# Optimization experiments

Measured on AMD Instinct MI355X. Metric: run time of the kernel, lower is better.

Reference implementation:

```python
import jax, jax.numpy as jnp
import numpy as np

N_NODES = 50000
N_EDGES = 600000
HIDDEN = 128
N_FEAT = 1
N_CLASSES = 2
N_GRAPHS = 500


def gcn_conv(x, W, b, src, dst, n_nodes):
    # PyG GCNConv: add self-loops, symmetric normalization deg^{-1/2} A_hat deg^{-1/2}, then XW + b
    h = x @ W  # [N, out]
    deg = jnp.zeros((n_nodes,), h.dtype).at[dst].add(1.0) + 1.0  # +1 for self-loop
    dinv = jax.lax.rsqrt(deg)
    norm = dinv[src] * dinv[dst]  # [E]
    agg = jax.ops.segment_sum(h[src] * norm[:, None], dst, num_segments=n_nodes)
    # self-loop contribution: norm_ii = dinv_i^2
    agg = agg + h * (dinv * dinv)[:, None]
    return agg + b


def setup_inputs() -> dict:
    key = jax.random.key(0)
    ks = jax.random.split(key, 12)
    x = jax.random.normal(ks[0], (N_NODES, N_FEAT), dtype=jnp.float32)
    edge_index = jax.random.randint(ks[1], (2, N_EDGES), 0, N_NODES, dtype=jnp.int64)
    batch = jnp.sort(jax.random.randint(ks[2], (N_NODES,), 0, N_GRAPHS, dtype=jnp.int64))

    def glorot(k, fan_in, fan_out):
        lim = np.sqrt(6.0 / (fan_in + fan_out)).astype(np.float32)
        return jax.random.uniform(k, (fan_in, fan_out), jnp.float32, -lim, lim)

    W1 = glorot(ks[3], N_FEAT, HIDDEN)
    b1 = jnp.zeros((HIDDEN,), jnp.float32)
    W2 = glorot(ks[4], HIDDEN, HIDDEN)
    b2 = jnp.zeros((HIDDEN,), jnp.float32)
    W3 = glorot(ks[5], HIDDEN, HIDDEN)
    b3 = jnp.zeros((HIDDEN,), jnp.float32)
    Wlin = glorot(ks[6], HIDDEN, N_CLASSES)
    blin = jnp.zeros((N_CLASSES,), jnp.float32)
    return {"x": x, "W1": W1, "b1": b1, "W2": W2, "b2": b2, "W3": W3,
            "b3": b3, "Wlin": Wlin, "blin": blin,
            "edge_index": edge_index, "batch": batch}


def reference(x, W1, b1, W2, b2, W3, b3, Wlin, blin, edge_index, batch):
    src, dst = edge_index[0], edge_index[1]
    n = x.shape[0]
    h = jax.nn.relu(gcn_conv(x, W1, b1, src, dst, n))
    h = jax.nn.relu(gcn_conv(h, W2, b2, src, dst, n))
    h = gcn_conv(h, W3, b3, src, dst, n)
    # global mean pool over graphs
    sums = jax.ops.segment_sum(h, batch, num_segments=N_GRAPHS)
    counts = jax.ops.segment_sum(jnp.ones((n,), h.dtype), batch, num_segments=N_GRAPHS)
    pooled = sums / jnp.maximum(counts, 1.0)[:, None]  # [G, HIDDEN]
    # dropout is identity in eval mode
    return pooled @ Wlin + blin  # [G, N_CLASSES]
```

## Files before the change

kernel.cpp:

```cpp
#include <hip/hip_runtime.h>

#define N_NODES 50000
#define N_EDGES 600000
#define HID     128
#define NG      500
#define MAXDEG  48
#define ECAP    664
#define NEB     147
#define NBUCK   782
#define BCAP    1024

typedef __attribute__((ext_vector_type(8))) short short8;
typedef __attribute__((ext_vector_type(4))) float f32x4;

static __device__ __forceinline__ ushort f2bf(float f) {
    uint u = __float_as_uint(f);
    return (ushort)((u + 0x7fffu + ((u >> 16) & 1u)) >> 16);
}
static __device__ __forceinline__ float bf2f(ushort h) {
    return __uint_as_float(((uint)h) << 16);
}


__global__ __launch_bounds__(256) void k_bin(const int* __restrict__ src,
                                             const int* __restrict__ dst,
                                             int* __restrict__ gcnt,
                                             uint* __restrict__ ebuf,
                                             const float* __restrict__ W2,
                                             const float* __restrict__ W3,
                                             const float* __restrict__ Wlin,
                                             const float* __restrict__ b3,
                                             const float* __restrict__ blin,
                                             const int* __restrict__ batch,
                                             float* __restrict__ w3buf,
                                             ushort* __restrict__ w2fh,
                                             ushort* __restrict__ w2fl,
                                             int* __restrict__ starts) {
    if (blockIdx.x >= NEB) {
        int t = threadIdx.x;
        if (blockIdx.x == NEB) {
            int k = t >> 1, j = t & 1;
            float acc = 0.f;
            for (int m = 0; m < 128; m++) acc += W3[k * 128 + m] * Wlin[m * 2 + j];
            w3buf[k * 2 + j] = acc;
            if (t < 2) {
                float c = 0.f;
                for (int m = 0; m < 128; m++) c += b3[m] * Wlin[m * 2 + t];
                w3buf[256 + t] = c + blin[t];
                w3buf[258 + t] = blin[t];
            }
            for (int g = t; g <= NG; g += 256) {
                int lo = 0, hi = N_NODES;
                while (lo < hi) { int mid = (lo + hi) >> 1; if (batch[mid] < g) lo = mid + 1; else hi = mid; }
                starts[g] = lo;
            }
        } else {
            int q = blockIdx.x - (NEB + 1);
            for (int idx = q * 4096 + t; idx < (q + 1) * 4096; idx += 256) {
                int nt = idx >> 11, kt = (idx >> 9) & 3, ln = (idx >> 3) & 63, i = idx & 7;
                int k = kt * 32 + (ln >> 4) * 8 + i;
                int col = nt * 16 + (ln & 15);
                float v = W2[k * 128 + col];
                ushort h = f2bf(v);
                w2fh[idx] = h;
                w2fl[idx] = f2bf(v - bf2f(h));
            }
        }
        return;
    }
    __shared__ int lcnt[NBUCK];
    __shared__ int gbase[NBUCK];
    int t = threadIdx.x;
    for (int i = t; i < NBUCK; i += 256) lcnt[i] = 0;
    __syncthreads();
    uint pk[16];
    uint blp[16];
    const int4* s4 = (const int4*)src;
    const int4* d4 = (const int4*)dst;
    int b4 = blockIdx.x * 1024;
    #pragma unroll
    for (int u = 0; u < 4; u++) {
        int i4 = b4 + u * 256 + t;
        if (i4 < N_EDGES / 4) {
            int4 dv = d4[i4], sv = s4[i4];
            int dd[4] = {dv.x, dv.y, dv.z, dv.w};
            int ss[4] = {sv.x, sv.y, sv.z, sv.w};
            #pragma unroll
            for (int j = 0; j < 4; j++) {
                int b = dd[j] >> 6;
                int p = atomicAdd(&lcnt[b], 1);
                pk[u * 4 + j]  = ((uint)ss[j] << 16) | (uint)(dd[j] & 63);
                blp[u * 4 + j] = ((uint)b << 12) | (uint)p;
            }
        } else {
            #pragma unroll
            for (int j = 0; j < 4; j++) blp[u * 4 + j] = 0xFFFFFFFFu;
        }
    }
    __syncthreads();
    for (int i = t; i < NBUCK; i += 256) {
        int c = lcnt[i];
        gbase[i] = c ? atomicAdd(&gcnt[i], c) : 0;
    }
    __syncthreads();
    #pragma unroll
    for (int u = 0; u < 16; u++) {
        if (blp[u] != 0xFFFFFFFFu) {
            int b = (int)(blp[u] >> 12);
            int slot = gbase[b] + (int)(blp[u] & 0xFFFu);
            if (slot < BCAP) ebuf[b * BCAP + slot] = pk[u];
        }
    }
}


__global__ __launch_bounds__(256) void k_place(const int* __restrict__ gcnt,
                                               const uint* __restrict__ ebuf,
                                               const float* __restrict__ x,
                                               int* __restrict__ ell,
                                               int* __restrict__ cnt,
                                               float* __restrict__ dinv,
                                               float* __restrict__ xd) {
    int b = blockIdx.x;
    __shared__ int lc[64];
    int t = threadIdx.x;
    if (t < 64) lc[t] = 0;
    __syncthreads();
    int n = min(gcnt[b], BCAP);
    int d0 = b << 6;
    for (int i = t; i < n; i += 256) {
        uint e = ebuf[b * BCAP + i];
        int dl = (int)(e & 63u);
        int s  = (int)(e >> 16);
        int p = atomicAdd(&lc[dl], 1);
        if (p < MAXDEG) ell[(d0 + dl) * MAXDEG + p] = s;
    }
    __syncthreads();
    if (t < 64) {
        int d = d0 + t;
        if (d < N_NODES) {
            int c = lc[t];
            cnt[d] = c;
            float di = rsqrtf((float)c + 1.0f);
            dinv[d] = di;
            xd[d] = x[d] * di;
        }
    }
}

__global__ void k_s1d(const float* __restrict__ xd, const float* __restrict__ dinv,
                      const int* __restrict__ cnt, const int* __restrict__ ell,
                      float2* __restrict__ s1d) {
    int tid = blockIdx.x * 256 + threadIdx.x;
    int i = tid >> 3, sub = tid & 7;
    if (i >= N_NODES) return;
    int c = min(cnt[i], MAXDEG);
    float acc = 0.f;
    for (int p = sub; p < c; p += 8) acc += xd[ell[i * MAXDEG + p]];
    acc += __shfl_xor(acc, 1);
    acc += __shfl_xor(acc, 2);
    acc += __shfl_xor(acc, 4);
    if (sub == 0) {
        float di = dinv[i];
        float2 r = {(xd[i] + acc) * di, di};
        s1d[i] = r;
    }
}


__global__ __launch_bounds__(256, 8) void k_gemm_fused(const float2* __restrict__ s1d,
                                                       const int* __restrict__ cnt,
                                                       const int* __restrict__ ell,
                                                       const float* __restrict__ W1,
                                                       const float* __restrict__ b1,
                                                       const ushort* __restrict__ w2fh,
                                                       const ushort* __restrict__ w2fl,
                                                       const float* __restrict__ b2,
                                                       const float* __restrict__ w3buf,
                                                       const float* __restrict__ dinv,
                                                       float* __restrict__ zd) {
    __shared__ __align__(16) ushort Hhi[32 * 136];
    __shared__ __align__(16) ushort Hlo[32 * 136];
    __shared__ float2 sjd_sh[ECAP];
    __shared__ int cnt_sh[32];
    __shared__ int pref_sh[33];
    int t = threadIdx.x;
    int r0 = blockIdx.x * 32;
    int lane = t & 31, grp = t >> 5;

    if (t < 32) {
        int i = r0 + t;
        int c = (i < N_NODES) ? min(cnt[i], MAXDEG) : 0;
        cnt_sh[t] = c;
        int inc = c;
        for (int o = 1; o < 32; o <<= 1) {
            int u = __shfl_up(inc, o);
            if (t >= o) inc += u;
        }
        pref_sh[t] = inc - c;
        if (t == 31) pref_sh[32] = inc;
    }
    __syncthreads();
    int total = pref_sh[32];
    bool fast = (total <= ECAP);
    if (fast) {
        #pragma unroll
        for (int u = 0; u < 6; u++) {
            int s = u * 256 + t;
            int ln = s / MAXDEG, p = s - ln * MAXDEG;
            if (p < cnt_sh[ln]) {
                int j = ell[(r0 + ln) * MAXDEG + p];
                sjd_sh[pref_sh[ln] + p] = s1d[j];
            }
        }
    }
    __syncthreads();

    float w1r[16], b1r[16];
    #pragma unroll
    for (int kk = 0; kk < 16; kk++) { w1r[kk] = W1[grp * 16 + kk]; b1r[kk] = b1[grp * 16 + kk]; }

    float ga[16];
    #pragma unroll
    for (int kk = 0; kk < 16; kk++) ga[kk] = 0.f;
    int node = r0 + lane;
    if (node < N_NODES) {
        float2 sd = s1d[node];
        float di = sd.y, wself = sd.y * sd.y;
        #pragma unroll
        for (int kk = 0; kk < 16; kk++) ga[kk] = fmaxf(sd.x * w1r[kk] + b1r[kk], 0.f) * wself;
        int c = cnt_sh[lane];
        if (fast) {
            const float2* myrow = &sjd_sh[pref_sh[lane]];
            int p = 0;
            for (; p + 3 < c; p += 4) {
                float2 s0 = myrow[p], s1v = myrow[p+1], s2 = myrow[p+2], s3 = myrow[p+3];
                float wj0 = s0.y * di, wj1 = s1v.y * di, wj2 = s2.y * di, wj3 = s3.y * di;
                #pragma unroll
                for (int kk = 0; kk < 16; kk++) {
                    ga[kk] += fmaxf(s0.x  * w1r[kk] + b1r[kk], 0.f) * wj0
                            + fmaxf(s1v.x * w1r[kk] + b1r[kk], 0.f) * wj1
                            + fmaxf(s2.x  * w1r[kk] + b1r[kk], 0.f) * wj2
                            + fmaxf(s3.x  * w1r[kk] + b1r[kk], 0.f) * wj3;
                }
            }
            for (; p < c; p++) {
                float2 sj = myrow[p];
                float wj = sj.y * di;
                #pragma unroll
                for (int kk = 0; kk < 16; kk++)
                    ga[kk] += fmaxf(sj.x * w1r[kk] + b1r[kk], 0.f) * wj;
            }
        } else {
            for (int p = 0; p < c; p++) {
                float2 sj = s1d[ell[node * MAXDEG + p]];
                float wj = sj.y * di;
                #pragma unroll
                for (int kk = 0; kk < 16; kk++)
                    ga[kk] += fmaxf(sj.x * w1r[kk] + b1r[kk], 0.f) * wj;
            }
        }
    }
    #pragma unroll
    for (int kk = 0; kk < 16; kk += 2) {
        int ch = grp * 16 + kk;
        ushort h0 = f2bf(ga[kk]);      ushort l0 = f2bf(ga[kk]     - bf2f(h0));
        ushort h1v = f2bf(ga[kk + 1]); ushort l1v = f2bf(ga[kk + 1] - bf2f(h1v));
        *(uint*)&Hhi[lane * 136 + ch] = (uint)h0 | ((uint)h1v << 16);
        *(uint*)&Hlo[lane * 136 + ch] = (uint)l0 | ((uint)l1v << 16);
    }
    __syncthreads();

    int wv = t >> 6, l = t & 63;
    int l15 = l & 15, lk = l >> 4;
    f32x4 acc00 = {0.f,0.f,0.f,0.f}, acc01 = {0.f,0.f,0.f,0.f};
    f32x4 acc10 = {0.f,0.f,0.f,0.f}, acc11 = {0.f,0.f,0.f,0.f};
    const short8* Bh = (const short8*)w2fh;
    const short8* Bl = (const short8*)w2fl;
    #pragma unroll
    for (int kt = 0; kt < 4; kt++) {
        int ao = l15 * 136 + kt * 32 + lk * 8;
        short8 ah0 = *(const short8*)&Hhi[ao];
        short8 ah1 = *(const short8*)&Hhi[ao + 16 * 136];
        short8 al0 = *(const short8*)&Hlo[ao];
        short8 al1 = *(const short8*)&Hlo[ao + 16 * 136];
        {
            int ng = 2 * wv;
            short8 bh = Bh[(ng * 4 + kt) * 64 + l];
            short8 bl = Bl[(ng * 4 + kt) * 64 + l];
            acc00 = __builtin_amdgcn_mfma_f32_16x16x32_bf16(ah0, bh, acc00, 0, 0, 0);
            acc00 = __builtin_amdgcn_mfma_f32_16x16x32_bf16(ah0, bl, acc00, 0, 0, 0);
            acc00 = __builtin_amdgcn_mfma_f32_16x16x32_bf16(al0, bh, acc00, 0, 0, 0);
            acc10 = __builtin_amdgcn_mfma_f32_16x16x32_bf16(ah1, bh, acc10, 0, 0, 0);
            acc10 = __builtin_amdgcn_mfma_f32_16x16x32_bf16(ah1, bl, acc10, 0, 0, 0);
            acc10 = __builtin_amdgcn_mfma_f32_16x16x32_bf16(al1, bh, acc10, 0, 0, 0);
        }
        {
            int ng = 2 * wv + 1;
            short8 bh = Bh[(ng * 4 + kt) * 64 + l];
            short8 bl = Bl[(ng * 4 + kt) * 64 + l];
            acc01 = __builtin_amdgcn_mfma_f32_16x16x32_bf16(ah0, bh, acc01, 0, 0, 0);
            acc01 = __builtin_amdgcn_mfma_f32_16x16x32_bf16(ah0, bl, acc01, 0, 0, 0);
            acc01 = __builtin_amdgcn_mfma_f32_16x16x32_bf16(al0, bh, acc01, 0, 0, 0);
            acc11 = __builtin_amdgcn_mfma_f32_16x16x32_bf16(ah1, bh, acc11, 0, 0, 0);
            acc11 = __builtin_amdgcn_mfma_f32_16x16x32_bf16(ah1, bl, acc11, 0, 0, 0);
            acc11 = __builtin_amdgcn_mfma_f32_16x16x32_bf16(al1, bh, acc11, 0, 0, 0);
        }
    }

    float p0[2][4], p1[2][4];
    #pragma unroll
    for (int mt = 0; mt < 2; mt++)
        #pragma unroll
        for (int r = 0; r < 4; r++) { p0[mt][r] = 0.f; p1[mt][r] = 0.f; }
    {
        int colg = (2 * wv) * 16 + l15;
        float b2c = b2[colg], w0 = w3buf[colg * 2], w1c = w3buf[colg * 2 + 1];
        #pragma unroll
        for (int r = 0; r < 4; r++) {
            float v0 = fmaxf(acc00[r] + b2c, 0.f);
            float v1 = fmaxf(acc10[r] + b2c, 0.f);
            p0[0][r] += v0 * w0; p1[0][r] += v0 * w1c;
            p0[1][r] += v1 * w0; p1[1][r] += v1 * w1c;
        }
    }
    {
        int colg = (2 * wv + 1) * 16 + l15;
        float b2c = b2[colg], w0 = w3buf[colg * 2], w1c = w3buf[colg * 2 + 1];
        #pragma unroll
        for (int r = 0; r < 4; r++) {
            float v0 = fmaxf(acc01[r] + b2c, 0.f);
            float v1 = fmaxf(acc11[r] + b2c, 0.f);
            p0[0][r] += v0 * w0; p1[0][r] += v0 * w1c;
            p0[1][r] += v1 * w0; p1[1][r] += v1 * w1c;
        }
    }
    #pragma unroll
    for (int o = 1; o < 16; o <<= 1) {
        #pragma unroll
        for (int mt = 0; mt < 2; mt++)
            #pragma unroll
            for (int r = 0; r < 4; r++) {
                p0[mt][r] += __shfl_xor(p0[mt][r], o);
                p1[mt][r] += __shfl_xor(p1[mt][r], o);
            }
    }
    float* zpart = (float*)sjd_sh;
    if (l15 == 0) {
        #pragma unroll
        for (int mt = 0; mt < 2; mt++)
            #pragma unroll
            for (int r = 0; r < 4; r++) {
                int row = mt * 16 + lk * 4 + r;
                zpart[(wv * 32 + row) * 2 + 0] = p0[mt][r];
                zpart[(wv * 32 + row) * 2 + 1] = p1[mt][r];
            }
    }
    __syncthreads();
    if (t < 64) {
        int row = t >> 1, o = t & 1;
        float s = zpart[row * 2 + o] + zpart[(32 + row) * 2 + o]
                + zpart[(64 + row) * 2 + o] + zpart[(96 + row) * 2 + o];
        int rg = r0 + row;
        if (rg < N_NODES) zd[rg * 2 + o] = s * dinv[rg];
    }
}


__global__ void k_aggz(const float* __restrict__ zd, const int* __restrict__ cnt,
                       const int* __restrict__ ell, const float* __restrict__ dinv,
                       const int* __restrict__ batch, float* __restrict__ gsum) {
    __shared__ float sa0[32], sa1[32];
    __shared__ int sg[32];
    int tid = blockIdx.x * 256 + threadIdx.x;
    int t = threadIdx.x;
    int i = tid >> 3, sub = tid & 7;
    const float2* Z = (const float2*)zd;
    float a0 = 0.f, a1 = 0.f;
    if (i < N_NODES) {
        int c = min(cnt[i], MAXDEG);
        for (int p = sub; p < c; p += 8) {
            float2 zj = Z[ell[i * MAXDEG + p]];
            a0 += zj.x; a1 += zj.y;
        }
    }
    a0 += __shfl_xor(a0, 1); a1 += __shfl_xor(a1, 1);
    a0 += __shfl_xor(a0, 2); a1 += __shfl_xor(a1, 2);
    a0 += __shfl_xor(a0, 4); a1 += __shfl_xor(a1, 4);
    if (sub == 0) {
        int li = t >> 3;
        if (i < N_NODES) {
            float di = dinv[i];
            float2 zi = Z[i];
            sa0[li] = (zi.x + a0) * di;
            sa1[li] = (zi.y + a1) * di;
            sg[li] = batch[i];
        } else { sa0[li] = 0.f; sa1[li] = 0.f; sg[li] = -1; }
    }
    __syncthreads();
    if (t < 32) {
        float v0 = sa0[t], v1 = sa1[t];
        int g = sg[t];
        #pragma unroll
        for (int o = 1; o < 32; o <<= 1) {
            float u0 = __shfl_up(v0, o), u1 = __shfl_up(v1, o);
            int ug = __shfl_up(g, o);
            if (t >= o && ug == g) { v0 += u0; v1 += u1; }
        }
        int gn = __shfl_down(g, 1);
        bool last = (t == 31) || (g != gn);
        if (last && g >= 0) {
            atomicAdd(&gsum[g * 2 + 0], v0);
            atomicAdd(&gsum[g * 2 + 1], v1);
        }
    }
}


__global__ __launch_bounds__(256) void k_final2(const float* __restrict__ gsum,
                                                const int* __restrict__ starts,
                                                const float* __restrict__ w3buf,
                                                float* __restrict__ out) {
    int t = threadIdx.x;
    for (int g = t; g < NG; g += 256) {
        int c = starts[g + 1] - starts[g];
        if (c > 0) {
            float inv = 1.0f / (float)c;
            out[g * 2 + 0] = gsum[g * 2 + 0] * inv + w3buf[256];
            out[g * 2 + 1] = gsum[g * 2 + 1] * inv + w3buf[257];
        } else {
            out[g * 2 + 0] = w3buf[258];
            out[g * 2 + 1] = w3buf[259];
        }
    }
}


extern "C" void kernel_launch(void* const* d_in, const int* in_sizes, int n_in,
                              void* d_out, int out_size, void* d_ws, size_t ws_size,
                              hipStream_t stream) {
    const float* x    = (const float*)d_in[0];
    const float* W1   = (const float*)d_in[1];
    const float* b1   = (const float*)d_in[2];
    const float* W2   = (const float*)d_in[3];
    const float* b2   = (const float*)d_in[4];
    const float* W3   = (const float*)d_in[5];
    const float* b3   = (const float*)d_in[6];
    const float* Wlin = (const float*)d_in[7];
    const float* blin = (const float*)d_in[8];
    const int*   eidx = (const int*)d_in[9];
    const int*   batch= (const int*)d_in[10];
    const int* esrc = eidx;
    const int* edst = eidx + N_EDGES;
    float* out = (float*)d_out;

    char* w = (char*)d_ws;
    size_t off = 0;
    auto alloc = [&](size_t bytes) { size_t o = off; off = (off + bytes + 255) & ~(size_t)255; return o; };
    int*   cnt    = (int*)  (w + alloc(N_NODES * 4));
    int*   ell    = (int*)  (w + alloc((size_t)N_NODES * MAXDEG * 4));
    float* dinv   = (float*)(w + alloc(N_NODES * 4));
    float* xd     = (float*)(w + alloc(N_NODES * 4));
    float2* s1d   = (float2*)(w + alloc((size_t)N_NODES * 8));
    float* w3buf  = (float*)(w + alloc(260 * 4));
    float* zd     = (float*)(w + alloc((size_t)N_NODES * 2 * 4));
    ushort* w2fh  = (ushort*)(w + alloc(16384 * 2));
    ushort* w2fl  = (ushort*)(w + alloc(16384 * 2));
    int*   starts = (int*)  (w + alloc((NG + 4) * 4));
    int*   gcnt   = (int*)  (w + alloc(NBUCK * 4));
    float* gsum   = (float*)(w + alloc(NG * 2 * 4));
    uint*  ebuf   = (uint*) (w + alloc((size_t)NBUCK * BCAP * 4));

    const int QB = (N_NODES * 8 + 255) / 256;
    size_t zbytes = (size_t)((char*)gsum - (char*)gcnt) + NG * 2 * 4;
    hipMemsetAsync(gcnt, 0, zbytes, stream);
    k_bin<<<NEB + 5, 256, 0, stream>>>(esrc, edst, gcnt, ebuf, W2, W3, Wlin, b3, blin,
                                       batch, w3buf, w2fh, w2fl, starts);
    k_place<<<NBUCK, 256, 0, stream>>>(gcnt, ebuf, x, ell, cnt, dinv, xd);
    k_s1d<<<QB, 256, 0, stream>>>(xd, dinv, cnt, ell, s1d);
    k_gemm_fused<<<(N_NODES + 31) / 32, 256, 0, stream>>>(s1d, cnt, ell,
                                                          W1, b1, w2fh, w2fl, b2, w3buf,
                                                          dinv, zd);
    k_aggz<<<QB, 256, 0, stream>>>(zd, cnt, ell, dinv, batch, gsum);
    k_final2<<<1, 256, 0, stream>>>(gsum, starts, w3buf, out);
}
```

Before: 145.6 us.

## Coarsen edge buckets to 512 nodes, stage-sort in LDS, fuse final into aggz

```diff
diff --git a/kernel.cpp b/kernel.cpp
--- a/kernel.cpp
+++ b/kernel.cpp
@@ -7,8 +7,8 @@
 #define MAXDEG  48
 #define ECAP    664
 #define NEB     147
-#define NBUCK   782
-#define BCAP    1024
+#define NBUCK   98
+#define BCAP    7168
 
 typedef __attribute__((ext_vector_type(8))) short short8;
 typedef __attribute__((ext_vector_type(4))) float f32x4;
@@ -68,13 +68,12 @@
         }
         return;
     }
-    __shared__ int lcnt[NBUCK];
-    __shared__ int gbase[NBUCK];
+    __shared__ int lcnt[NBUCK], lexc[NBUCK], lpos[NBUCK], gbase[NBUCK];
+    __shared__ uint lrec[4096];
     int t = threadIdx.x;
-    for (int i = t; i < NBUCK; i += 256) lcnt[i] = 0;
+    if (t < NBUCK) lcnt[t] = 0;
     __syncthreads();
     uint pk[16];
-    uint blp[16];
     const int4* s4 = (const int4*)src;
     const int4* d4 = (const int4*)dst;
     int b4 = blockIdx.x * 1024;
@@ -87,29 +86,47 @@
             int ss[4] = {sv.x, sv.y, sv.z, sv.w};
             #pragma unroll
             for (int j = 0; j < 4; j++) {
-                int b = dd[j] >> 6;
-                int p = atomicAdd(&lcnt[b], 1);
-                pk[u * 4 + j]  = ((uint)ss[j] << 16) | (uint)(dd[j] & 63);
-                blp[u * 4 + j] = ((uint)b << 12) | (uint)p;
+                pk[u * 4 + j] = ((uint)ss[j] << 16) | (uint)dd[j];
+                atomicAdd(&lcnt[dd[j] >> 9], 1);
             }
         } else {
             #pragma unroll
-            for (int j = 0; j < 4; j++) blp[u * 4 + j] = 0xFFFFFFFFu;
-        }
-    }
-    __syncthreads();
-    for (int i = t; i < NBUCK; i += 256) {
-        int c = lcnt[i];
-        gbase[i] = c ? atomicAdd(&gcnt[i], c) : 0;
+            for (int j = 0; j < 4; j++) pk[u * 4 + j] = 0xFFFFFFFFu;
+        }
+    }
+    __syncthreads();
+    if (t < NBUCK) lexc[t] = lcnt[t];
+    __syncthreads();
+    for (int o = 1; o < NBUCK; o <<= 1) {
+        int v = (t < NBUCK && t >= o) ? lexc[t - o] : 0;
+        __syncthreads();
+        if (t < NBUCK) lexc[t] += v;
+        __syncthreads();
+    }
+    if (t < NBUCK) {
+        int c = lcnt[t];
+        int e = lexc[t] - c;
+        lexc[t] = e;
+        lpos[t] = e;
+        gbase[t] = c ? atomicAdd(&gcnt[t], c) : 0;
     }
     __syncthreads();
     #pragma unroll
     for (int u = 0; u < 16; u++) {
-        if (blp[u] != 0xFFFFFFFFu) {
-            int b = (int)(blp[u] >> 12);
-            int slot = gbase[b] + (int)(blp[u] & 0xFFFu);
-            if (slot < BCAP) ebuf[b * BCAP + slot] = pk[u];
-        }
+        uint r = pk[u];
+        if (r != 0xFFFFFFFFu) {
+            int b = (int)((r & 0xFFFFu) >> 9);
+            int p = atomicAdd(&lpos[b], 1);
+            lrec[p] = r;
+        }
+    }
+    __syncthreads();
+    int total = lexc[NBUCK - 1] + lcnt[NBUCK - 1];
+    for (int s = t; s < total; s += 256) {
+        uint r = lrec[s];
+        int b = (int)((r & 0xFFFFu) >> 9);
+        int gi = gbase[b] + (s - lexc[b]);
+        if (gi < BCAP) ebuf[b * BCAP + gi] = r;
     }
 }
 
@@ -122,24 +139,25 @@
                                                float* __restrict__ dinv,
                                                float* __restrict__ xd) {
     int b = blockIdx.x;
-    __shared__ int lc[64];
+    __shared__ int lc[512];
     int t = threadIdx.x;
-    if (t < 64) lc[t] = 0;
+    lc[t] = 0; lc[t + 256] = 0;
     __syncthreads();
     int n = min(gcnt[b], BCAP);
-    int d0 = b << 6;
+    int d0 = b << 9;
     for (int i = t; i < n; i += 256) {
         uint e = ebuf[b * BCAP + i];
-        int dl = (int)(e & 63u);
-        int s  = (int)(e >> 16);
+        int dl = (int)(e & 511u);
         int p = atomicAdd(&lc[dl], 1);
-        if (p < MAXDEG) ell[(d0 + dl) * MAXDEG + p] = s;
-    }
-    __syncthreads();
-    if (t < 64) {
-        int d = d0 + t;
+        if (p < MAXDEG) ell[(d0 + dl) * MAXDEG + p] = (int)(e >> 16);
+    }
+    __syncthreads();
+    #pragma unroll
+    for (int u = 0; u < 2; u++) {
+        int dl = u * 256 + t;
+        int d = d0 + dl;
         if (d < N_NODES) {
-            int c = lc[t];
+            int c = lc[dl];
             cnt[d] = c;
             float di = rsqrtf((float)c + 1.0f);
             dinv[d] = di;
@@ -369,9 +387,12 @@
 
 __global__ void k_aggz(const float* __restrict__ zd, const int* __restrict__ cnt,
                        const int* __restrict__ ell, const float* __restrict__ dinv,
-                       const int* __restrict__ batch, float* __restrict__ gsum) {
+                       const int* __restrict__ batch, float* __restrict__ gsum,
+                       int* __restrict__ done, const int* __restrict__ starts,
+                       const float* __restrict__ w3buf, float* __restrict__ out) {
     __shared__ float sa0[32], sa1[32];
     __shared__ int sg[32];
+    __shared__ int lastf;
     int tid = blockIdx.x * 256 + threadIdx.x;
     int t = threadIdx.x;
     int i = tid >> 3, sub = tid & 7;
@@ -414,23 +435,24 @@
             atomicAdd(&gsum[g * 2 + 1], v1);
         }
     }
-}
-
-
-__global__ __launch_bounds__(256) void k_final2(const float* __restrict__ gsum,
-                                                const int* __restrict__ starts,
-                                                const float* __restrict__ w3buf,
-                                                float* __restrict__ out) {
-    int t = threadIdx.x;
-    for (int g = t; g < NG; g += 256) {
-        int c = starts[g + 1] - starts[g];
-        if (c > 0) {
-            float inv = 1.0f / (float)c;
-            out[g * 2 + 0] = gsum[g * 2 + 0] * inv + w3buf[256];
-            out[g * 2 + 1] = gsum[g * 2 + 1] * inv + w3buf[257];
-        } else {
-            out[g * 2 + 0] = w3buf[258];
-            out[g * 2 + 1] = w3buf[259];
+    if (t == 0) {
+        __threadfence();
+        lastf = (atomicAdd(done, 1) == (int)gridDim.x - 1) ? 1 : 0;
+    }
+    __syncthreads();
+    if (lastf) {
+        for (int g = t; g < NG; g += 256) {
+            float s0 = atomicAdd(&gsum[g * 2 + 0], 0.0f);
+            float s1v = atomicAdd(&gsum[g * 2 + 1], 0.0f);
+            int c = starts[g + 1] - starts[g];
+            if (c > 0) {
+                float inv = 1.0f / (float)c;
+                out[g * 2 + 0] = s0 * inv + w3buf[256];
+                out[g * 2 + 1] = s1v * inv + w3buf[257];
+            } else {
+                out[g * 2 + 0] = w3buf[258];
+                out[g * 2 + 1] = w3buf[259];
+            }
         }
     }
 }
@@ -467,13 +489,13 @@
     ushort* w2fh  = (ushort*)(w + alloc(16384 * 2));
     ushort* w2fl  = (ushort*)(w + alloc(16384 * 2));
     int*   starts = (int*)  (w + alloc((NG + 4) * 4));
-    int*   gcnt   = (int*)  (w + alloc(NBUCK * 4));
+    int*   gcnt   = (int*)  (w + alloc(128 * 4));
     float* gsum   = (float*)(w + alloc(NG * 2 * 4));
     uint*  ebuf   = (uint*) (w + alloc((size_t)NBUCK * BCAP * 4));
+    int*   done   = gcnt + 112;
 
     const int QB = (N_NODES * 8 + 255) / 256;
-    size_t zbytes = (size_t)((char*)gsum - (char*)gcnt) + NG * 2 * 4;
-    hipMemsetAsync(gcnt, 0, zbytes, stream);
+    hipMemsetAsync(gcnt, 0, 128 * 4 + NG * 2 * 4, stream);
     k_bin<<<NEB + 5, 256, 0, stream>>>(esrc, edst, gcnt, ebuf, W2, W3, Wlin, b3, blin,
                                        batch, w3buf, w2fh, w2fl, starts);
     k_place<<<NBUCK, 256, 0, stream>>>(gcnt, ebuf, x, ell, cnt, dinv, xd);
@@ -481,6 +503,6 @@
     k_gemm_fused<<<(N_NODES + 31) / 32, 256, 0, stream>>>(s1d, cnt, ell,
                                                           W1, b1, w2fh, w2fl, b2, w3buf,
                                                           dinv, zd);
-    k_aggz<<<QB, 256, 0, stream>>>(zd, cnt, ell, dinv, batch, gsum);
-    k_final2<<<1, 256, 0, stream>>>(gsum, starts, w3buf, out);
-}
+    k_aggz<<<QB, 256, 0, stream>>>(zd, cnt, ell, dinv, batch, gsum,
+                                   done, starts, w3buf, out);
+}
```

After: 182.0 us. 25.0% more time.

## Double rows per block in fused GEMM and fold final kernel into aggregation

Applied to the files above, without the earlier changes.

```diff
diff --git a/kernel.cpp b/kernel.cpp
--- a/kernel.cpp
+++ b/kernel.cpp
@@ -5,10 +5,10 @@
 #define HID     128
 #define NG      500
 #define MAXDEG  48
-#define ECAP    664
 #define NEB     147
 #define NBUCK   782
 #define BCAP    1024
+#define ECAP2   2176
 
 typedef __attribute__((ext_vector_type(8))) short short8;
 typedef __attribute__((ext_vector_type(4))) float f32x4;
@@ -19,6 +19,9 @@
 }
 static __device__ __forceinline__ float bf2f(ushort h) {
     return __uint_as_float(((uint)h) << 16);
+}
+static __device__ __forceinline__ float rfl(float v) {
+    return __uint_as_float(__builtin_amdgcn_readfirstlane(__float_as_uint(v)));
 }
 
 
@@ -131,9 +134,8 @@
     for (int i = t; i < n; i += 256) {
         uint e = ebuf[b * BCAP + i];
         int dl = (int)(e & 63u);
-        int s  = (int)(e >> 16);
         int p = atomicAdd(&lc[dl], 1);
-        if (p < MAXDEG) ell[(d0 + dl) * MAXDEG + p] = s;
+        if (p < MAXDEG) ell[(d0 + dl) * MAXDEG + p] = (int)(e >> 16);
     }
     __syncthreads();
     if (t < 64) {
@@ -168,7 +170,7 @@
 }
 
 
-__global__ __launch_bounds__(256, 8) void k_gemm_fused(const float2* __restrict__ s1d,
+__global__ __launch_bounds__(512, 8) void k_gemm_fused(const float2* __restrict__ s1d,
                                                        const int* __restrict__ cnt,
                                                        const int* __restrict__ ell,
                                                        const float* __restrict__ W1,
@@ -179,34 +181,36 @@
                                                        const float* __restrict__ w3buf,
                                                        const float* __restrict__ dinv,
                                                        float* __restrict__ zd) {
-    __shared__ __align__(16) ushort Hhi[32 * 136];
-    __shared__ __align__(16) ushort Hlo[32 * 136];
-    __shared__ float2 sjd_sh[ECAP];
-    __shared__ int cnt_sh[32];
-    __shared__ int pref_sh[33];
+    __shared__ __align__(16) ushort Hhi[64 * 136];
+    __shared__ __align__(16) ushort Hlo[64 * 136];
+    __shared__ int cnt_sh[64];
+    __shared__ int pref_sh[65];
+    float2* sjd_sh = (float2*)Hlo;
+    float*  zpart  = (float*)Hhi;
+
     int t = threadIdx.x;
-    int r0 = blockIdx.x * 32;
-    int lane = t & 31, grp = t >> 5;
-
-    if (t < 32) {
+    int r0 = blockIdx.x * 64;
+    int row = t & 63, grp = t >> 6;
+
+    if (t < 64) {
         int i = r0 + t;
         int c = (i < N_NODES) ? min(cnt[i], MAXDEG) : 0;
         cnt_sh[t] = c;
         int inc = c;
-        for (int o = 1; o < 32; o <<= 1) {
+        for (int o = 1; o < 64; o <<= 1) {
             int u = __shfl_up(inc, o);
             if (t >= o) inc += u;
         }
         pref_sh[t] = inc - c;
-        if (t == 31) pref_sh[32] = inc;
-    }
-    __syncthreads();
-    int total = pref_sh[32];
-    bool fast = (total <= ECAP);
+        if (t == 63) pref_sh[64] = inc;
+    }
+    __syncthreads();
+    int total = pref_sh[64];
+    bool fast = (total <= ECAP2);
     if (fast) {
         #pragma unroll
         for (int u = 0; u < 6; u++) {
-            int s = u * 256 + t;
+            int s = u * 512 + t;
             int ln = s / MAXDEG, p = s - ln * MAXDEG;
             if (p < cnt_sh[ln]) {
                 int j = ell[(r0 + ln) * MAXDEG + p];
@@ -218,20 +222,23 @@
 
     float w1r[16], b1r[16];
     #pragma unroll
-    for (int kk = 0; kk < 16; kk++) { w1r[kk] = W1[grp * 16 + kk]; b1r[kk] = b1[grp * 16 + kk]; }
+    for (int kk = 0; kk < 16; kk++) {
+        w1r[kk] = rfl(W1[grp * 16 + kk]);
+        b1r[kk] = rfl(b1[grp * 16 + kk]);
+    }
 
     float ga[16];
     #pragma unroll
     for (int kk = 0; kk < 16; kk++) ga[kk] = 0.f;
-    int node = r0 + lane;
+    int node = r0 + row;
     if (node < N_NODES) {
         float2 sd = s1d[node];
         float di = sd.y, wself = sd.y * sd.y;
         #pragma unroll
         for (int kk = 0; kk < 16; kk++) ga[kk] = fmaxf(sd.x * w1r[kk] + b1r[kk], 0.f) * wself;
-        int c = cnt_sh[lane];
+        int c = cnt_sh[row];
         if (fast) {
-            const float2* myrow = &sjd_sh[pref_sh[lane]];
+            const float2* myrow = &sjd_sh[pref_sh[row]];
             int p = 0;
             for (; p + 3 < c; p += 4) {
                 float2 s0 = myrow[p], s1v = myrow[p+1], s2 = myrow[p+2], s3 = myrow[p+3];
@@ -261,107 +268,86 @@
             }
         }
     }
+    __syncthreads();
+
     #pragma unroll
     for (int kk = 0; kk < 16; kk += 2) {
         int ch = grp * 16 + kk;
         ushort h0 = f2bf(ga[kk]);      ushort l0 = f2bf(ga[kk]     - bf2f(h0));
         ushort h1v = f2bf(ga[kk + 1]); ushort l1v = f2bf(ga[kk + 1] - bf2f(h1v));
-        *(uint*)&Hhi[lane * 136 + ch] = (uint)h0 | ((uint)h1v << 16);
-        *(uint*)&Hlo[lane * 136 + ch] = (uint)l0 | ((uint)l1v << 16);
-    }
-    __syncthreads();
-
-    int wv = t >> 6, l = t & 63;
-    int l15 = l & 15, lk = l >> 4;
-    f32x4 acc00 = {0.f,0.f,0.f,0.f}, acc01 = {0.f,0.f,0.f,0.f};
-    f32x4 acc10 = {0.f,0.f,0.f,0.f}, acc11 = {0.f,0.f,0.f,0.f};
+        *(uint*)&Hhi[row * 136 + ch] = (uint)h0 | ((uint)h1v << 16);
+        *(uint*)&Hlo[row * 136 + ch] = (uint)l0 | ((uint)l1v << 16);
+    }
+    __syncthreads();
+
+    int l = t & 63, l15 = l & 15, lk = l >> 4;
+    f32x4 acc0 = {0.f,0.f,0.f,0.f}, acc1 = {0.f,0.f,0.f,0.f};
+    f32x4 acc2 = {0.f,0.f,0.f,0.f}, acc3 = {0.f,0.f,0.f,0.f};
     const short8* Bh = (const short8*)w2fh;
     const short8* Bl = (const short8*)w2fl;
     #pragma unroll
     for (int kt = 0; kt < 4; kt++) {
+        short8 bh = Bh[(grp * 4 + kt) * 64 + l];
+        short8 bl = Bl[(grp * 4 + kt) * 64 + l];
         int ao = l15 * 136 + kt * 32 + lk * 8;
-        short8 ah0 = *(const short8*)&Hhi[ao];
-        short8 ah1 = *(const short8*)&Hhi[ao + 16 * 136];
-        short8 al0 = *(const short8*)&Hlo[ao];
-        short8 al1 = *(const short8*)&Hlo[ao + 16 * 136];
-        {
-            int ng = 2 * wv;
-            short8 bh = Bh[(ng * 4 + kt) * 64 + l];
-            short8 bl = Bl[(ng * 4 + kt) * 64 + l];
-            acc00 = __builtin_amdgcn_mfma_f32_16x16x32_bf16(ah0, bh, acc00, 0, 0, 0);
-            acc00 = __builtin_amdgcn_mfma_f32_16x16x32_bf16(ah0, bl, acc00, 0, 0, 0);
-            acc00 = __builtin_amdgcn_mfma_f32_16x16x32_bf16(al0, bh, acc00, 0, 0, 0);
-            acc10 = __builtin_amdgcn_mfma_f32_16x16x32_bf16(ah1, bh, acc10, 0, 0, 0);
-            acc10 = __builtin_amdgcn_mfma_f32_16x16x32_bf16(ah1, bl, acc10, 0, 0, 0);
-            acc10 = __builtin_amdgcn_mfma_f32_16x16x32_bf16(al1, bh, acc10, 0, 0, 0);
-        }
-        {
-            int ng = 2 * wv + 1;
-            short8 bh = Bh[(ng * 4 + kt) * 64 + l];
-            short8 bl = Bl[(ng * 4 + kt) * 64 + l];
-            acc01 = __builtin_amdgcn_mfma_f32_16x16x32_bf16(ah0, bh, acc01, 0, 0, 0);
-            acc01 = __builtin_amdgcn_mfma_f32_16x16x32_bf16(ah0, bl, acc01, 0, 0, 0);
-            acc01 = __builtin_amdgcn_mfma_f32_16x16x32_bf16(al0, bh, acc01, 0, 0, 0);
-            acc11 = __builtin_amdgcn_mfma_f32_16x16x32_bf16(ah1, bh, acc11, 0, 0, 0);
-            acc11 = __builtin_amdgcn_mfma_f32_16x16x32_bf16(ah1, bl, acc11, 0, 0, 0);
-            acc11 = __builtin_amdgcn_mfma_f32_16x16x32_bf16(al1, bh, acc11, 0, 0, 0);
-        }
-    }
-
-    float p0[2][4], p1[2][4];
-    #pragma unroll
-    for (int mt = 0; mt < 2; mt++)
-        #pragma unroll
-        for (int r = 0; r < 4; r++) { p0[mt][r] = 0.f; p1[mt][r] = 0.f; }
-    {
-        int colg = (2 * wv) * 16 + l15;
-        float b2c = b2[colg], w0 = w3buf[colg * 2], w1c = w3buf[colg * 2 + 1];
+        {   short8 ah = *(const short8*)&Hhi[ao];
+            short8 al = *(const short8*)&Hlo[ao];
+            acc0 = __builtin_amdgcn_mfma_f32_16x16x32_bf16(ah, bh, acc0, 0, 0, 0);
+            acc0 = __builtin_amdgcn_mfma_f32_16x16x32_bf16(ah, bl, acc0, 0, 0, 0);
+            acc0 = __builtin_amdgcn_mfma_f32_16x16x32_bf16(al, bh, acc0, 0, 0, 0); }
+        {   short8 ah = *(const short8*)&Hhi[ao + 16 * 136];
+            short8 al = *(const short8*)&Hlo[ao + 16 * 136];
+            acc1 = __builtin_amdgcn_mfma_f32_16x16x32_bf16(ah, bh, acc1, 0, 0, 0);
+            acc1 = __builtin_amdgcn_mfma_f32_16x16x32_bf16(ah, bl, acc1, 0, 0, 0);
+            acc1 = __builtin_amdgcn_mfma_f32_16x16x32_bf16(al, bh, acc1, 0, 0, 0); }
+        {   short8 ah = *(const short8*)&Hhi[ao + 32 * 136];
+            short8 al = *(const short8*)&Hlo[ao + 32 * 136];
+            acc2 = __builtin_amdgcn_mfma_f32_16x16x32_bf16(ah, bh, acc2, 0, 0, 0);
+            acc2 = __builtin_amdgcn_mfma_f32_16x16x32_bf16(ah, bl, acc2, 0, 0, 0);
+            acc2 = __builtin_amdgcn_mfma_f32_16x16x32_bf16(al, bh, acc2, 0, 0, 0); }
+        {   short8 ah = *(const short8*)&Hhi[ao + 48 * 136];
+            short8 al = *(const short8*)&Hlo[ao + 48 * 136];
+            acc3 = __builtin_amdgcn_mfma_f32_16x16x32_bf16(ah, bh, acc3, 0, 0, 0);
+            acc3 = __builtin_amdgcn_mfma_f32_16x16x32_bf16(ah, bl, acc3, 0, 0, 0);
+            acc3 = __builtin_amdgcn_mfma_f32_16x16x32_bf16(al, bh, acc3, 0, 0, 0); }
+    }
+    __syncthreads();
+
+    int colg = grp * 16 + l15;
+    float b2c = b2[colg], w0 = w3buf[colg * 2], w1c = w3buf[colg * 2 + 1];
+    #pragma unroll
+    for (int mt = 0; mt < 4; mt++) {
+        f32x4 a = (mt == 0) ? acc0 : (mt == 1) ? acc1 : (mt == 2) ? acc2 : acc3;
+        float q0[4], q1[4];
         #pragma unroll
         for (int r = 0; r < 4; r++) {
-            float v0 = fmaxf(acc00[r] + b2c, 0.f);
-            float v1 = fmaxf(acc10[r] + b2c, 0.f);
-            p0[0][r] += v0 * w0; p1[0][r] += v0 * w1c;
-            p0[1][r] += v1 * w0; p1[1][r] += v1 * w1c;
-        }
-    }
-    {
-        int colg = (2 * wv + 1) * 16 + l15;
-        float b2c = b2[colg], w0 = w3buf[colg * 2], w1c = w3buf[colg * 2 + 1];
-        #pragma unroll
-        for (int r = 0; r < 4; r++) {
-            float v0 = fmaxf(acc01[r] + b2c, 0.f);
-            float v1 = fmaxf(acc11[r] + b2c, 0.f);
-            p0[0][r] += v0 * w0; p1[0][r] += v0 * w1c;
-            p0[1][r] += v1 * w0; p1[1][r] += v1 * w1c;
-        }
-    }
-    #pragma unroll
-    for (int o = 1; o < 16; o <<= 1) {
-        #pragma unroll
-        for (int mt = 0; mt < 2; mt++)
+            float v = fmaxf(a[r] + b2c, 0.f);
+            q0[r] = v * w0; q1[r] = v * w1c;
+        }
+        #pragma unroll
+        for (int o = 1; o < 16; o <<= 1) {
             #pragma unroll
             for (int r = 0; r < 4; r++) {
-                p0[mt][r] += __shfl_xor(p0[mt][r], o);
-                p1[mt][r] += __shfl_xor(p1[mt][r], o);
-            }
-    }
-    float* zpart = (float*)sjd_sh;
-    if (l15 == 0) {
-        #pragma unroll
-        for (int mt = 0; mt < 2; mt++)
+                q0[r] += __shfl_xor(q0[r], o);
+                q1[r] += __shfl_xor(q1[r], o);
+            }
+        }
+        if (l15 == 0) {
             #pragma unroll
             for (int r = 0; r < 4; r++) {
-                int row = mt * 16 + lk * 4 + r;
-                zpart[(wv * 32 + row) * 2 + 0] = p0[mt][r];
-                zpart[(wv * 32 + row) * 2 + 1] = p1[mt][r];
-            }
-    }
-    __syncthreads();
-    if (t < 64) {
-        int row = t >> 1, o = t & 1;
-        float s = zpart[row * 2 + o] + zpart[(32 + row) * 2 + o]
-                + zpart[(64 + row) * 2 + o] + zpart[(96 + row) * 2 + o];
-        int rg = r0 + row;
+                int rl = mt * 16 + lk * 4 + r;
+                zpart[(grp * 64 + rl) * 2 + 0] = q0[r];
+                zpart[(grp * 64 + rl) * 2 + 1] = q1[r];
+            }
+        }
+    }
+    __syncthreads();
+    if (t < 128) {
+        int rl = t >> 1, o = t & 1;
+        float s = 0.f;
+        #pragma unroll
+        for (int w = 0; w < 8; w++) s += zpart[(w * 64 + rl) * 2 + o];
+        int rg = r0 + rl;
         if (rg < N_NODES) zd[rg * 2 + o] = s * dinv[rg];
     }
 }
@@ -369,9 +355,12 @@
 
 __global__ void k_aggz(const float* __restrict__ zd, const int* __restrict__ cnt,
                        const int* __restrict__ ell, const float* __restrict__ dinv,
-                       const int* __restrict__ batch, float* __restrict__ gsum) {
+                       const int* __restrict__ batch, float* __restrict__ gsum,
+                       int* __restrict__ done, const int* __restrict__ starts,
+                       const float* __restrict__ w3buf, float* __restrict__ out) {
     __shared__ float sa0[32], sa1[32];
     __shared__ int sg[32];
+    __shared__ int lastf;
     int tid = blockIdx.x * 256 + threadIdx.x;
     int t = threadIdx.x;
     int i = tid >> 3, sub = tid & 7;
@@ -414,23 +403,24 @@
             atomicAdd(&gsum[g * 2 + 1], v1);
         }
     }
-}
-
-
-__global__ __launch_bounds__(256) void k_final2(const float* __restrict__ gsum,
-                                                const int* __restrict__ starts,
-                                                const float* __restrict__ w3buf,
-                                                float* __restrict__ out) {
-    int t = threadIdx.x;
-    for (int g = t; g < NG; g += 256) {
-        int c = starts[g + 1] - starts[g];
-        if (c > 0) {
-            float inv = 1.0f / (float)c;
-            out[g * 2 + 0] = gsum[g * 2 + 0] * inv + w3buf[256];
-            out[g * 2 + 1] = gsum[g * 2 + 1] * inv + w3buf[257];
-        } else {
-            out[g * 2 + 0] = w3buf[258];
-            out[g * 2 + 1] = w3buf[259];
+    if (t == 0) {
+        __threadfence();
+        lastf = (atomicAdd(done, 1) == (int)gridDim.x - 1) ? 1 : 0;
+    }
+    __syncthreads();
+    if (lastf) {
+        for (int g = t; g < NG; g += 256) {
+            float s0 = atomicAdd(&gsum[g * 2 + 0], 0.0f);
+            float s1v = atomicAdd(&gsum[g * 2 + 1], 0.0f);
+            int c = starts[g + 1] - starts[g];
+            if (c > 0) {
+                float inv = 1.0f / (float)c;
+                out[g * 2 + 0] = s0 * inv + w3buf[256];
+                out[g * 2 + 1] = s1v * inv + w3buf[257];
+            } else {
+                out[g * 2 + 0] = w3buf[258];
+                out[g * 2 + 1] = w3buf[259];
+            }
         }
     }
 }
@@ -467,20 +457,20 @@
     ushort* w2fh  = (ushort*)(w + alloc(16384 * 2));
     ushort* w2fl  = (ushort*)(w + alloc(16384 * 2));
     int*   starts = (int*)  (w + alloc((NG + 4) * 4));
-    int*   gcnt   = (int*)  (w + alloc(NBUCK * 4));
+    int*   gcnt   = (int*)  (w + alloc(1024 * 4));
     float* gsum   = (float*)(w + alloc(NG * 2 * 4));
     uint*  ebuf   = (uint*) (w + alloc((size_t)NBUCK * BCAP * 4));
+    int*   done   = gcnt + 800;
 
     const int QB = (N_NODES * 8 + 255) / 256;
-    size_t zbytes = (size_t)((char*)gsum - (char*)gcnt) + NG * 2 * 4;
-    hipMemsetAsync(gcnt, 0, zbytes, stream);
+    hipMemsetAsync(gcnt, 0, 1024 * 4 + NG * 2 * 4, stream);
     k_bin<<<NEB + 5, 256, 0, stream>>>(esrc, edst, gcnt, ebuf, W2, W3, Wlin, b3, blin,
                                        batch, w3buf, w2fh, w2fl, starts);
     k_place<<<NBUCK, 256, 0, stream>>>(gcnt, ebuf, x, ell, cnt, dinv, xd);
     k_s1d<<<QB, 256, 0, stream>>>(xd, dinv, cnt, ell, s1d);
-    k_gemm_fused<<<(N_NODES + 31) / 32, 256, 0, stream>>>(s1d, cnt, ell,
+    k_gemm_fused<<<(N_NODES + 63) / 64, 512, 0, stream>>>(s1d, cnt, ell,
                                                           W1, b1, w2fh, w2fl, b2, w3buf,
                                                           dinv, zd);
-    k_aggz<<<QB, 256, 0, stream>>>(zd, cnt, ell, dinv, batch, gsum);
-    k_final2<<<1, 256, 0, stream>>>(gsum, starts, w3buf, out);
-}
+    k_aggz<<<QB, 256, 0, stream>>>(zd, cnt, ell, dinv, batch, gsum,
+                                   done, starts, w3buf, out);
+}
```

Result: slower. 271.4 us (+86.4%).
